# Optimization experiments

Hardware: AMD Instinct MI355X
Metric: run time of the kernel (lower is better)

Reference implementation:

```python
import jax, jax.numpy as jnp
import numpy as np

KSIZE = 7   # pooled output grid (kernel_size)
SR = 2      # bilinear sampling ratio per bin side


def setup_inputs() -> dict:
    key = jax.random.key(0)
    k1, k2, k3 = jax.random.split(key, 3)
    B, H, W, C = 8, 64, 64, 256
    N = 4096
    x = jax.random.normal(k1, (B, H, W, C), jnp.float32)
    # random valid boxes in feature-map coordinates: (y1, x1, y2, x2), y2 > y1
    raw = jax.random.uniform(k2, (N, 4), jnp.float32)
    c1 = raw[:, :2] * jnp.array([H - 1.0, W - 1.0], jnp.float32)
    c2 = raw[:, 2:] * jnp.array([H - 1.0, W - 1.0], jnp.float32)
    lo = jnp.minimum(c1, c2)
    hi = jnp.maximum(c1, c2) + 1.0  # ensure non-degenerate boxes
    rois = jnp.stack([lo[:, 0], lo[:, 1], hi[:, 0], hi[:, 1]], axis=1)
    batch_idx = jax.random.randint(k3, (N,), 0, B, jnp.int32)
    return {"x": x, "rois": rois, "batch_idx": batch_idx}


def reference(x, rois, batch_idx):
    """ROIAlign: per-ROI bilinear sampling + average pooling.

    x:         [B, H, W, C] feature map (channels-last)
    rois:      [N, 4] boxes (y1, x1, y2, x2) in feature-map pixel coords
    batch_idx: [N] int index of the image each ROI belongs to
    returns:   [N, KSIZE, KSIZE, C]
    """
    B, H, W, C = x.shape
    N = rois.shape[0]
    K, S = KSIZE, KSIZE * SR  # S x S sample points per ROI

    y1, x1, y2, x2 = rois[:, 0], rois[:, 1], rois[:, 2], rois[:, 3]
    bin_h = (y2 - y1) / K
    bin_w = (x2 - x1) / K

    # sample coordinate s within ROI: y1 + (s + 0.5)/SR * bin_h, s in [0, S)
    off = (jnp.arange(S, dtype=x.dtype) + 0.5) / SR          # [S]
    sy = y1[:, None] + off[None, :] * bin_h[:, None]          # [N, S]
    sx = x1[:, None] + off[None, :] * bin_w[:, None]          # [N, S]

    yy = sy[:, :, None]                                       # [N, S, 1]
    xx = sx[:, None, :]                                       # [N, 1, S]
    y0 = jnp.clip(jnp.floor(yy), 0, H - 2).astype(jnp.int32)  # [N, S, 1]
    x0 = jnp.clip(jnp.floor(xx), 0, W - 2).astype(jnp.int32)  # [N, 1, S]
    ly = jnp.clip(yy - y0, 0.0, 1.0)                          # [N, S, 1]
    lx = jnp.clip(xx - x0, 0.0, 1.0)                          # [N, 1, S]

    b = batch_idx[:, None, None]                              # [N, 1, 1]
    # gather 4 bilinear corners -> each [N, S, S, C]
    v00 = x[b, y0, x0]
    v01 = x[b, y0, x0 + 1]
    v10 = x[b, y0 + 1, x0]
    v11 = x[b, y0 + 1, x0 + 1]

    ly_ = ly[..., None]  # [N, S, 1, 1]
    lx_ = lx[..., None]  # [N, 1, S, 1]
    val = (v00 * (1 - ly_) * (1 - lx_) + v01 * (1 - ly_) * lx_
           + v10 * ly_ * (1 - lx_) + v11 * ly_ * lx_)          # [N, S, S, C]

    # average-pool the SR x SR samples inside each of the K x K bins
    out = val.reshape(N, K, SR, K, SR, C).mean(axis=(2, 4))   # [N, K, K, C]
    return out
```

## Files before the change

kernel.cpp:

```cpp
#include <hip/hip_runtime.h>

#define KSIZE 7
#define SR    2
#define SAMP  (KSIZE * SR)
#define NBINS (KSIZE * KSIZE)
#define NMAX  4096
#define BMAX  8

typedef float v4f __attribute__((ext_vector_type(4)));

constexpr int C4c  = 64;
constexpr int WC4c = 4096;

__global__ __launch_bounds__(256) void bucket_kernel(
    const int* __restrict__ bi, int* __restrict__ assign, int N, int B, int cap)
{
    __shared__ int cnt[BMAX];
    __shared__ int ovf_n, ovf_c;
    __shared__ int asg[NMAX];
    __shared__ int ovf[NMAX];

    const int t = threadIdx.x;
    if (t < BMAX) cnt[t] = 0;
    if (t == 0) { ovf_n = 0; ovf_c = 0; }
    for (int i = t; i < N; i += 256) asg[i] = -1;
    __syncthreads();

    for (int i = t; i < N; i += 256) {
        int k = bi[i];
        int p = atomicAdd(&cnt[k], 1);
        if (p < cap) asg[p * B + k] = i;
        else { int q = atomicAdd(&ovf_n, 1); ovf[q] = i; }
    }
    __syncthreads();

    for (int i = t; i < N; i += 256) {
        if (asg[i] < 0) { int q = atomicAdd(&ovf_c, 1); asg[i] = ovf[q]; }
    }
    __syncthreads();

    for (int i = t; i < N; i += 256) assign[i] = asg[i];
}

__device__ __forceinline__ void issue_bin(
    v4f (&V)[16], int bin, const v4f* __restrict__ xbase,
    const int* y0s, const int* x0s)
{
    const int ky  = bin / KSIZE;
    const int kx  = bin - ky * KSIZE;
    const int ya0 = y0s[ky * SR], ya1 = y0s[ky * SR + 1];
    const int xa0 = x0s[kx * SR], xa1 = x0s[kx * SR + 1];
    const v4f* q0 = xbase + ya0 * WC4c + xa0 * C4c;
    const v4f* q1 = xbase + ya0 * WC4c + xa1 * C4c;
    const v4f* q2 = xbase + ya1 * WC4c + xa0 * C4c;
    const v4f* q3 = xbase + ya1 * WC4c + xa1 * C4c;
    V[0]  = q0[0]; V[1]  = q0[C4c]; V[2]  = q0[WC4c]; V[3]  = q0[WC4c + C4c];
    V[4]  = q1[0]; V[5]  = q1[C4c]; V[6]  = q1[WC4c]; V[7]  = q1[WC4c + C4c];
    V[8]  = q2[0]; V[9]  = q2[C4c]; V[10] = q2[WC4c]; V[11] = q2[WC4c + C4c];
    V[12] = q3[0]; V[13] = q3[C4c]; V[14] = q3[WC4c]; V[15] = q3[WC4c + C4c];
}

__device__ __forceinline__ void compute_bin(
    const v4f (&V)[16], int bin, float* __restrict__ outn, int lane,
    const float* lys, const float* lxs)
{
    const int ky = bin / KSIZE;
    const int kx = bin - ky * KSIZE;
    v4f acc = {0.f, 0.f, 0.f, 0.f};
    #pragma unroll
    for (int s = 0; s < 4; ++s) {
        const float ly  = lys[ky * SR + (s >> 1)];
        const float lx  = lxs[kx * SR + (s & 1)];
        const float w00 = (1.f - ly) * (1.f - lx);
        const float w01 = (1.f - ly) * lx;
        const float w10 = ly * (1.f - lx);
        const float w11 = ly * lx;
        acc += V[4*s+0]*w00 + V[4*s+1]*w01 + V[4*s+2]*w10 + V[4*s+3]*w11;
    }
    acc *= 0.25f;
    v4f* op = (v4f*)(outn + (size_t)bin * 256) + lane;
    __builtin_nontemporal_store(acc, op);
}

__global__ __launch_bounds__(256, 3) void roialign_kernel(
    const float* __restrict__ x,
    const float* __restrict__ rois,
    const int*   __restrict__ batch_idx,
    float*       __restrict__ out,
    const int*   __restrict__ assign,
    int H, int W, int C)
{
    __shared__ int   sh_n;
    __shared__ int   y0s[SAMP];
    __shared__ float lys[SAMP];
    __shared__ int   x0s[SAMP];
    __shared__ float lxs[SAMP];

    const int t = threadIdx.x;
    if (t == 0) sh_n = assign[blockIdx.x];
    __syncthreads();
    const int n = sh_n;

    const float4 rb = ((const float4*)rois)[n];
    const float bin_h = (rb.z - rb.x) / (float)KSIZE;
    const float bin_w = (rb.w - rb.y) / (float)KSIZE;

    if (t < SAMP) {
        const float off = ((float)t + 0.5f) / (float)SR;
        const float sy  = rb.x + off * bin_h;
        float fy = floorf(sy);
        fy = fminf(fmaxf(fy, 0.0f), (float)(H - 2));
        y0s[t] = (int)fy;
        lys[t] = fminf(fmaxf(sy - fy, 0.0f), 1.0f);
    } else if (t < 2 * SAMP) {
        const int s = t - SAMP;
        const float off = ((float)s + 0.5f) / (float)SR;
        const float sx  = rb.y + off * bin_w;
        float fx = floorf(sx);
        fx = fminf(fmaxf(fx, 0.0f), (float)(W - 2));
        x0s[s] = (int)fx;
        lxs[s] = fminf(fmaxf(sx - fx, 0.0f), 1.0f);
    }
    __syncthreads();

    const int bimg = batch_idx[n];
    const int lane = t & 63;
    const int wave = t >> 6;

    const v4f* __restrict__ xbase =
        (const v4f*)x + (size_t)bimg * 64 * WC4c + lane;
    float* __restrict__ outn = out + (size_t)n * NBINS * 256;

    v4f vA[16], vB[16];

    int bin = wave;
    issue_bin(vA, bin, xbase, y0s, x0s);
    for (;;) {
        int nb = bin + 4;
        if (nb < NBINS) {
            issue_bin(vB, nb, xbase, y0s, x0s);
            compute_bin(vA, bin, outn, lane, lys, lxs);
            bin = nb;
        } else {
            compute_bin(vA, bin, outn, lane, lys, lxs);
            break;
        }
        nb = bin + 4;
        if (nb < NBINS) {
            issue_bin(vA, nb, xbase, y0s, x0s);
            compute_bin(vB, bin, outn, lane, lys, lxs);
            bin = nb;
        } else {
            compute_bin(vB, bin, outn, lane, lys, lxs);
            break;
        }
    }
}

extern "C" void kernel_launch(void* const* d_in, const int* in_sizes, int n_in,
                              void* d_out, int out_size, void* d_ws, size_t ws_size,
                              hipStream_t stream) {
    const float* x         = (const float*)d_in[0];
    const float* rois      = (const float*)d_in[1];
    const int*   batch_idx = (const int*)d_in[2];
    float*       out       = (float*)d_out;
    int*         assign    = (int*)d_ws;

    const int H = 64, W = 64, C = 256;
    const int N = in_sizes[1] / 4;
    const int B = in_sizes[0] / (H * W * C);
    const int cap = N / B;

    bucket_kernel<<<1, 256, 0, stream>>>(batch_idx, assign, N, B, cap);
    roialign_kernel<<<N, 256, 0, stream>>>(x, rois, batch_idx, out, assign,
                                           H, W, C);
}
```

Baseline: 312.4 us.

## Precompute separable per-bin row/column tap indices and weights with duplicate-tap merging

Replaces per-sample bilinear corner loads with a separable formulation. Each bin row and column now gets four distinct tap indices and combined weights, with the 0.5 averaging folded in. When the two samples in a bin share or abut a pixel, the duplicate taps are merged and padded with zero-weight entries that point at an already-loaded address. The loads still number 16 per bin, but overlapping taps now hit the same address, so cache traffic can drop. The weight math moves from per-bin work into a small per-ROI table.

```diff
diff --git a/kernel.cpp b/kernel.cpp
--- a/kernel.cpp
+++ b/kernel.cpp
@@ -2,7 +2,6 @@
 
 #define KSIZE 7
 #define SR    2
-#define SAMP  (KSIZE * SR)
 #define NBINS (KSIZE * KSIZE)
 #define NMAX  4096
 #define BMAX  8
@@ -42,46 +41,6 @@
     for (int i = t; i < N; i += 256) assign[i] = asg[i];
 }
 
-__device__ __forceinline__ void issue_bin(
-    v4f (&V)[16], int bin, const v4f* __restrict__ xbase,
-    const int* y0s, const int* x0s)
-{
-    const int ky  = bin / KSIZE;
-    const int kx  = bin - ky * KSIZE;
-    const int ya0 = y0s[ky * SR], ya1 = y0s[ky * SR + 1];
-    const int xa0 = x0s[kx * SR], xa1 = x0s[kx * SR + 1];
-    const v4f* q0 = xbase + ya0 * WC4c + xa0 * C4c;
-    const v4f* q1 = xbase + ya0 * WC4c + xa1 * C4c;
-    const v4f* q2 = xbase + ya1 * WC4c + xa0 * C4c;
-    const v4f* q3 = xbase + ya1 * WC4c + xa1 * C4c;
-    V[0]  = q0[0]; V[1]  = q0[C4c]; V[2]  = q0[WC4c]; V[3]  = q0[WC4c + C4c];
-    V[4]  = q1[0]; V[5]  = q1[C4c]; V[6]  = q1[WC4c]; V[7]  = q1[WC4c + C4c];
-    V[8]  = q2[0]; V[9]  = q2[C4c]; V[10] = q2[WC4c]; V[11] = q2[WC4c + C4c];
-    V[12] = q3[0]; V[13] = q3[C4c]; V[14] = q3[WC4c]; V[15] = q3[WC4c + C4c];
-}
-
-__device__ __forceinline__ void compute_bin(
-    const v4f (&V)[16], int bin, float* __restrict__ outn, int lane,
-    const float* lys, const float* lxs)
-{
-    const int ky = bin / KSIZE;
-    const int kx = bin - ky * KSIZE;
-    v4f acc = {0.f, 0.f, 0.f, 0.f};
-    #pragma unroll
-    for (int s = 0; s < 4; ++s) {
-        const float ly  = lys[ky * SR + (s >> 1)];
-        const float lx  = lxs[kx * SR + (s & 1)];
-        const float w00 = (1.f - ly) * (1.f - lx);
-        const float w01 = (1.f - ly) * lx;
-        const float w10 = ly * (1.f - lx);
-        const float w11 = ly * lx;
-        acc += V[4*s+0]*w00 + V[4*s+1]*w01 + V[4*s+2]*w10 + V[4*s+3]*w11;
-    }
-    acc *= 0.25f;
-    v4f* op = (v4f*)(outn + (size_t)bin * 256) + lane;
-    __builtin_nontemporal_store(acc, op);
-}
-
 __global__ __launch_bounds__(256, 3) void roialign_kernel(
     const float* __restrict__ x,
     const float* __restrict__ rois,
@@ -91,10 +50,10 @@
     int H, int W, int C)
 {
     __shared__ int   sh_n;
-    __shared__ int   y0s[SAMP];
-    __shared__ float lys[SAMP];
-    __shared__ int   x0s[SAMP];
-    __shared__ float lxs[SAMP];
+    __shared__ int   ridx[KSIZE][4];
+    __shared__ float rwgt[KSIZE][4];
+    __shared__ int   cidx[KSIZE][4];
+    __shared__ float cwgt[KSIZE][4];
 
     const int t = threadIdx.x;
     if (t == 0) sh_n = assign[blockIdx.x];
@@ -105,21 +64,43 @@
     const float bin_h = (rb.z - rb.x) / (float)KSIZE;
     const float bin_w = (rb.w - rb.y) / (float)KSIZE;
 
-    if (t < SAMP) {
-        const float off = ((float)t + 0.5f) / (float)SR;
-        const float sy  = rb.x + off * bin_h;
-        float fy = floorf(sy);
-        fy = fminf(fmaxf(fy, 0.0f), (float)(H - 2));
-        y0s[t] = (int)fy;
-        lys[t] = fminf(fmaxf(sy - fy, 0.0f), 1.0f);
-    } else if (t < 2 * SAMP) {
-        const int s = t - SAMP;
-        const float off = ((float)s + 0.5f) / (float)SR;
-        const float sx  = rb.y + off * bin_w;
-        float fx = floorf(sx);
-        fx = fminf(fmaxf(fx, 0.0f), (float)(W - 2));
-        x0s[s] = (int)fx;
-        lxs[s] = fminf(fmaxf(sx - fx, 0.0f), 1.0f);
+    if (t < KSIZE || (t >= 16 && t < 16 + KSIZE)) {
+        const bool isrow = (t < KSIZE);
+        const int  k     = isrow ? t : t - 16;
+        const float base = isrow ? rb.x : rb.y;
+        const float bsz  = isrow ? bin_h : bin_w;
+        const int   dim  = isrow ? H : W;
+
+        const float sA = base + ((float)k + 0.25f) * bsz;
+        const float sB = base + ((float)k + 0.75f) * bsz;
+        const float fA = fminf(fmaxf(floorf(sA), 0.0f), (float)(dim - 2));
+        const float fB = fminf(fmaxf(floorf(sB), 0.0f), (float)(dim - 2));
+        const int   iA = (int)fA,  iB = (int)fB;
+        const float lA = fminf(fmaxf(sA - fA, 0.0f), 1.0f);
+        const float lB = fminf(fmaxf(sB - fB, 0.0f), 1.0f);
+
+        int   i0 = iA,     i1 = iA + 1, i2, i3;
+        float w0 = (1.0f - lA) * 0.5f, w1 = lA * 0.5f, w2, w3;
+        if (iB == iA) {
+            w0 += (1.0f - lB) * 0.5f;
+            w1 += lB * 0.5f;
+            i2 = iA; w2 = 0.0f;
+            i3 = iA; w3 = 0.0f;
+        } else if (iB == iA + 1) {
+            w1 += (1.0f - lB) * 0.5f;
+            i2 = iB + 1; w2 = lB * 0.5f;
+            i3 = iA;     w3 = 0.0f;
+        } else {
+            i2 = iB;     w2 = (1.0f - lB) * 0.5f;
+            i3 = iB + 1; w3 = lB * 0.5f;
+        }
+        if (isrow) {
+            ridx[k][0] = i0; ridx[k][1] = i1; ridx[k][2] = i2; ridx[k][3] = i3;
+            rwgt[k][0] = w0; rwgt[k][1] = w1; rwgt[k][2] = w2; rwgt[k][3] = w3;
+        } else {
+            cidx[k][0] = i0; cidx[k][1] = i1; cidx[k][2] = i2; cidx[k][3] = i3;
+            cwgt[k][0] = w0; cwgt[k][1] = w1; cwgt[k][2] = w2; cwgt[k][3] = w3;
+        }
     }
     __syncthreads();
 
@@ -133,28 +114,63 @@
 
     v4f vA[16], vB[16];
 
+#define ISSUE(V, KY, KX)                                                    \
+    do {                                                                    \
+        const v4f* r0_ = xbase + ridx[KY][0] * WC4c;                        \
+        const v4f* r1_ = xbase + ridx[KY][1] * WC4c;                        \
+        const v4f* r2_ = xbase + ridx[KY][2] * WC4c;                        \
+        const v4f* r3_ = xbase + ridx[KY][3] * WC4c;                        \
+        const int c0_ = cidx[KX][0] * C4c, c1_ = cidx[KX][1] * C4c;         \
+        const int c2_ = cidx[KX][2] * C4c, c3_ = cidx[KX][3] * C4c;         \
+        V[0]  = r0_[c0_]; V[1]  = r0_[c1_]; V[2]  = r0_[c2_]; V[3]  = r0_[c3_]; \
+        V[4]  = r1_[c0_]; V[5]  = r1_[c1_]; V[6]  = r1_[c2_]; V[7]  = r1_[c3_]; \
+        V[8]  = r2_[c0_]; V[9]  = r2_[c1_]; V[10] = r2_[c2_]; V[11] = r2_[c3_]; \
+        V[12] = r3_[c0_]; V[13] = r3_[c1_]; V[14] = r3_[c2_]; V[15] = r3_[c3_]; \
+    } while (0)
+
+#define COMPUTE(V, BIN, KY, KX)                                             \
+    do {                                                                    \
+        v4f acc = {0.f, 0.f, 0.f, 0.f};                                     \
+        _Pragma("unroll")                                                   \
+        for (int r_ = 0; r_ < 4; ++r_) {                                    \
+            const float wr_ = rwgt[KY][r_];                                 \
+            acc += V[r_*4+0] * (wr_ * cwgt[KX][0]);                         \
+            acc += V[r_*4+1] * (wr_ * cwgt[KX][1]);                         \
+            acc += V[r_*4+2] * (wr_ * cwgt[KX][2]);                         \
+            acc += V[r_*4+3] * (wr_ * cwgt[KX][3]);                         \
+        }                                                                   \
+        v4f* op_ = (v4f*)(outn + (size_t)(BIN) * 256) + lane;               \
+        __builtin_nontemporal_store(acc, op_);                              \
+    } while (0)
+
     int bin = wave;
-    issue_bin(vA, bin, xbase, y0s, x0s);
+    int kyA = bin / KSIZE, kxA = bin - kyA * KSIZE;
+    int kyB, kxB;
+    ISSUE(vA, kyA, kxA);
     for (;;) {
         int nb = bin + 4;
         if (nb < NBINS) {
-            issue_bin(vB, nb, xbase, y0s, x0s);
-            compute_bin(vA, bin, outn, lane, lys, lxs);
+            kyB = nb / KSIZE; kxB = nb - kyB * KSIZE;
+            ISSUE(vB, kyB, kxB);
+            COMPUTE(vA, bin, kyA, kxA);
             bin = nb;
         } else {
-            compute_bin(vA, bin, outn, lane, lys, lxs);
+            COMPUTE(vA, bin, kyA, kxA);
             break;
         }
         nb = bin + 4;
         if (nb < NBINS) {
-            issue_bin(vA, nb, xbase, y0s, x0s);
-            compute_bin(vB, bin, outn, lane, lys, lxs);
+            kyA = nb / KSIZE; kxA = nb - kyA * KSIZE;
+            ISSUE(vA, kyA, kxA);
+            COMPUTE(vB, bin, kyB, kxB);
             bin = nb;
         } else {
-            compute_bin(vB, bin, outn, lane, lys, lxs);
+            COMPUTE(vB, bin, kyB, kxB);
             break;
         }
     }
+#undef ISSUE
+#undef COMPUTE
 }
 
 extern "C" void kernel_launch(void* const* d_in, const int* in_sizes, int n_in,
```

Measured after the change: 314.4 us. No clear change (+0.6%).
